# Performance work log

Hardware: AMD Instinct MI355X
Metric: run time of the kernel (lower is better)

## Reference

```python
import jax, jax.numpy as jnp
import numpy as np

B, DIM, N = 4, 256, 2048
DIM_CTX, M = 256, 2048
HEADS, DIM_HEAD = 8, 64
DIM_INNER = HEADS * DIM_HEAD  # 512
EPS = 1e-12  # matches F.normalize eps


def setup_inputs() -> dict:
    key = jax.random.key(0)
    ks = jax.random.split(key, 8)
    return {
        "fmap": jax.random.normal(ks[0], (B, DIM, N), dtype=jnp.float32),
        "context": jax.random.normal(ks[1], (B, DIM_CTX, M), dtype=jnp.float32),
        "mask": jax.random.randint(ks[2], (B, M), 0, 2) > 0,
        "gamma": jnp.ones((DIM, 1), dtype=jnp.float32),
        "gamma_ctx": jnp.ones((DIM_CTX, 1), dtype=jnp.float32),
        "Wq": jax.random.normal(ks[3], (DIM_INNER, DIM), dtype=jnp.float32) * (DIM ** -0.5),
        "Wkv": jax.random.normal(ks[4], (2 * DIM_INNER, DIM_CTX), dtype=jnp.float32) * (DIM_CTX ** -0.5),
        "Wout": jax.random.normal(ks[5], (DIM, DIM_INNER), dtype=jnp.float32) * (DIM_INNER ** -0.5),
    }


def channel_rmsnorm(x, gamma):
    # F.normalize(x, dim=1) * sqrt(dim) * gamma ; x: [b, c, n], gamma: [c, 1]
    scale = x.shape[1] ** 0.5
    norm = jnp.sqrt(jnp.sum(x * x, axis=1, keepdims=True))
    normed = x / jnp.maximum(norm, EPS)
    return normed * scale * gamma[None]


def reference(fmap, context, mask, gamma, gamma_ctx, Wq, Wkv, Wout):
    h, d = HEADS, DIM_HEAD
    attn_scale = d ** -0.5

    fmap_n = channel_rmsnorm(fmap, gamma)          # [b, dim, n]
    ctx_n = channel_rmsnorm(context, gamma_ctx)    # [b, dim_ctx, m]

    # 1x1 Conv1d == matmul over channels
    q = jnp.einsum('oc,bcn->bon', Wq, fmap_n)      # [b, h*d, n]
    kv = jnp.einsum('oc,bcm->bom', Wkv, ctx_n)     # [b, 2*h*d, m]
    k, v = jnp.split(kv, 2, axis=1)

    # [b, h*d, n] -> [b, h, n, d]
    def to_heads(t):
        b, _, nn = t.shape
        return t.reshape(b, h, d, nn).transpose(0, 1, 3, 2)

    q, k, v = to_heads(q), to_heads(k), to_heads(v)

    # L2-distance attention: sim = -||q_i - k_j||_2 * scale
    q2 = jnp.sum(q * q, axis=-1)                   # [b, h, n]
    k2 = jnp.sum(k * k, axis=-1)                   # [b, h, m]
    qk = jnp.einsum('bhid,bhjd->bhij', q, k)       # [b, h, n, m]
    d2 = jnp.maximum(q2[..., :, None] + k2[..., None, :] - 2.0 * qk, 0.0)
    dist = jnp.sqrt(jnp.maximum(d2, EPS))
    sim = -dist * attn_scale

    neg_max = -jnp.finfo(sim.dtype).max
    sim = jnp.where(mask[:, None, None, :], sim, neg_max)

    attn = jax.nn.softmax(sim, axis=-1)            # [b, h, n, m]
    out = jnp.einsum('bhij,bhjd->bhid', attn, v)   # [b, h, n, d]
    out = out.transpose(0, 1, 3, 2).reshape(out.shape[0], h * d, -1)  # [b, h*d, n]
    return jnp.einsum('oc,bcn->bon', Wout, out)    # [b, dim, n]
```

## Files before the change

### kernel.cpp

```cpp
#include <hip/hip_runtime.h>
#include <hip/hip_bf16.h>

#define B_ 4
#define DIM_ 256
#define N_ 2048
#define M_ 2048
#define HEADS_ 8
#define DHEAD_ 64
#define DINNER_ 512

typedef __attribute__((ext_vector_type(8))) short short8;
typedef __attribute__((ext_vector_type(4))) short short4v;
typedef __attribute__((ext_vector_type(4))) float floatx4;
typedef __attribute__((ext_vector_type(4))) _Float16 half4;
typedef __attribute__((ext_vector_type(8))) _Float16 half8;

#if defined(__has_builtin)
#if __has_builtin(__builtin_amdgcn_global_load_lds)
#define HAS_DMA 1
#endif
#endif

typedef __attribute__((address_space(1))) const void gvoid_t;
typedef __attribute__((address_space(3))) void lvoid_t;

#define CQ_ 0.18033688011112042f
#define NEG2CQ_ (-0.36067376022224084f)
#define EPS2_ 3.25213893e-14f

__device__ inline short bf16r(float x) {
  unsigned u = __float_as_uint(x);
  unsigned r = (u + 0x7fffu + ((u >> 16) & 1u)) >> 16;
  return (short)r;
}
__device__ inline float bf2f(short b) {
  return __uint_as_float(((unsigned)(unsigned short)b) << 16);
}

__global__ __launch_bounds__(256) void preproc_kernel(
    const float* __restrict__ Wq, const float* __restrict__ Wkv,
    const float* __restrict__ Wout, const float* __restrict__ gamma,
    const float* __restrict__ gctx, short* __restrict__ whi,
    short* __restrict__ wlo, const float* __restrict__ xf,
    const float* __restrict__ xc, short* __restrict__ xtf,
    short* __restrict__ xtc) {
  const int bid = blockIdx.x;
  const int tid = threadIdx.x;

  __shared__ float4 red4[16][16];
  __shared__ float scl[64];
  __shared__ float t[64][65];

  if (bid < 768) {
    const int y = bid >> 8;
    const int gsz[3] = {32768, 65536, 32768};
    const int goff[3] = {0, 131072, 393216};
    int gidx = (bid & 255) * 256 + tid;
    if (gidx >= gsz[y]) return;
    const float* W = (y == 0) ? Wq : (y == 1) ? Wkv : Wout;
    const int cmask = (y == 2) ? 511 : 255;
    int e0 = gidx * 4;
    int c = e0 & cmask;
    float4 wv = *(const float4*)&W[e0];
    if (y < 2) {
      const float* g = (y == 0) ? gamma : gctx;
      float4 g4 = *(const float4*)&g[c];
      wv.x *= g4.x; wv.y *= g4.y; wv.z *= g4.z; wv.w *= g4.w;
    }
    float vv[4] = {wv.x, wv.y, wv.z, wv.w};
    short4v hi, lo;
#pragma unroll
    for (int e = 0; e < 4; ++e) {
      short hb = bf16r(vv[e]);
      hi[e] = hb;
      lo[e] = bf16r(vv[e] - bf2f(hb));
    }
    *(short4v*)&whi[goff[y] + e0] = hi;
    *(short4v*)&wlo[goff[y] + e0] = lo;
    return;
  }

  const int cid = bid - 768;
  const int NN = 2048;
  const int z = cid >> 7;
  const int b = (cid >> 5) & 3;
  const int xblk = cid & 31;
  const float* x = (z == 0) ? xf : xc;
  short* xt = (z == 0) ? xtf : xtc;
  const int tx4 = tid & 15, tyc = tid >> 4;
  const int n0 = xblk * 64;
  const float* xb = x + (size_t)b * 256 * NN;

  float4 ssq4 = {0.f, 0.f, 0.f, 0.f};
  for (int c = tyc; c < 256; c += 16) {
    float4 v = *(const float4*)&xb[(size_t)c * NN + n0 + tx4 * 4];
    ssq4.x += v.x * v.x; ssq4.y += v.y * v.y;
    ssq4.z += v.z * v.z; ssq4.w += v.w * v.w;
  }
  red4[tyc][tx4] = ssq4;
  __syncthreads();
  if (tid < 16) {
    float4 s = red4[0][tid];
#pragma unroll
    for (int g = 1; g < 16; ++g) {
      float4 v = red4[g][tid];
      s.x += v.x; s.y += v.y; s.z += v.z; s.w += v.w;
    }
    scl[tid * 4 + 0] = 16.0f / fmaxf(sqrtf(s.x), 1e-12f);
    scl[tid * 4 + 1] = 16.0f / fmaxf(sqrtf(s.y), 1e-12f);
    scl[tid * 4 + 2] = 16.0f / fmaxf(sqrtf(s.z), 1e-12f);
    scl[tid * 4 + 3] = 16.0f / fmaxf(sqrtf(s.w), 1e-12f);
  }
  const int row = tid >> 2, cg = tid & 3;
  for (int c0 = 0; c0 < 256; c0 += 64) {
    __syncthreads();
    for (int cc = tyc; cc < 64; cc += 16) {
      float4 v = *(const float4*)&xb[(size_t)(c0 + cc) * NN + n0 + tx4 * 4];
      t[cc][tx4 * 4 + 0] = v.x;
      t[cc][tx4 * 4 + 1] = v.y;
      t[cc][tx4 * 4 + 2] = v.z;
      t[cc][tx4 * 4 + 3] = v.w;
    }
    __syncthreads();
    float sc = scl[row];
    short8 o0v, o1v;
#pragma unroll
    for (int e = 0; e < 8; ++e) {
      o0v[e] = bf16r(t[cg * 16 + e][row] * sc);
      o1v[e] = bf16r(t[cg * 16 + 8 + e][row] * sc);
    }
    size_t base = ((size_t)b * NN + n0 + row) * 256 + c0 + cg * 16;
    *(short8*)&xt[base] = o0v;
    *(short8*)&xt[base + 8] = o1v;
  }
}

__global__ __launch_bounds__(256) void qkv_gemm_kernel(
    const short* __restrict__ whi, const short* __restrict__ wlo,
    const short* __restrict__ fmap_t, const short* __restrict__ ctx_t,
    short* __restrict__ qb, short* __restrict__ kc, _Float16* __restrict__ vc,
    const int* __restrict__ maskp, float* __restrict__ k2m) {
  const int b = blockIdx.z;
  const int y = blockIdx.y;
  const bool isq = (y < 4);
  const int o0 = (isq ? y : y - 4) * 128;
  const int n0 = blockIdx.x * 128;
  const short* Wh = whi + (isq ? 0 : 131072);
  const short* Wl = wlo + (isq ? 0 : 131072);
  const short* Xt = isq ? fmap_t : ctx_t;

  const int tid = threadIdx.x;
  const int w = tid >> 6, l = tid & 63, quad = l >> 4, l15 = l & 15;
  const int wo = (w >> 1) * 64, wn = (w & 1) * 64;

  __shared__ __align__(16) char smem[36864];
  short* lWh = (short*)smem;
  short* lWl = (short*)(smem + 8192);
  short* lXb = (short*)(smem + 16384);

  floatx4 acc[4][4];
#pragma unroll
  for (int ot = 0; ot < 4; ++ot)
#pragma unroll
    for (int nt = 0; nt < 4; ++nt)
#pragma unroll
      for (int r = 0; r < 4; ++r) acc[ot][nt][r] = 0.f;

  const int drow = l >> 2;
  const int dslot = l & 3;

  for (int c0 = 0; c0 < 256; c0 += 32) {
    __syncthreads();
#pragma unroll
    for (int half = 0; half < 2; ++half) {
      int r0 = w * 32 + half * 16;
      int row = r0 + drow;
      int chunk = dslot ^ ((row >> 1) & 3);
      size_t wsrc = (size_t)(o0 + row) * 256 + c0 + chunk * 8;
      size_t xsrc = ((size_t)b * 2048 + n0 + row) * 256 + c0 + chunk * 8;
#ifdef HAS_DMA
      __builtin_amdgcn_global_load_lds((gvoid_t*)&Wh[wsrc],
                                       (lvoid_t*)&lWh[r0 * 32], 16, 0, 0);
      __builtin_amdgcn_global_load_lds((gvoid_t*)&Wl[wsrc],
                                       (lvoid_t*)&lWl[r0 * 32], 16, 0, 0);
      __builtin_amdgcn_global_load_lds((gvoid_t*)&Xt[xsrc],
                                       (lvoid_t*)&lXb[r0 * 32], 16, 0, 0);
#else
      *(short8*)&lWh[row * 32 + dslot * 8] = *(const short8*)&Wh[wsrc];
      *(short8*)&lWl[row * 32 + dslot * 8] = *(const short8*)&Wl[wsrc];
      *(short8*)&lXb[row * 32 + dslot * 8] = *(const short8*)&Xt[xsrc];
#endif
    }
    __syncthreads();

    short8 ah[4], al[4], bx[4];
#pragma unroll
    for (int ot = 0; ot < 4; ++ot) {
      int ar = wo + 16 * ot + l15;
      int sl = (quad ^ ((ar >> 1) & 3)) * 8;
      ah[ot] = *(const short8*)&lWh[ar * 32 + sl];
      al[ot] = *(const short8*)&lWl[ar * 32 + sl];
    }
#pragma unroll
    for (int nt = 0; nt < 4; ++nt) {
      int br = wn + 16 * nt + l15;
      int sl = (quad ^ ((br >> 1) & 3)) * 8;
      bx[nt] = *(const short8*)&lXb[br * 32 + sl];
    }
#pragma unroll
    for (int ot = 0; ot < 4; ++ot)
#pragma unroll
      for (int nt = 0; nt < 4; ++nt) {
        acc[ot][nt] =
            __builtin_amdgcn_mfma_f32_16x16x32_bf16(al[ot], bx[nt], acc[ot][nt], 0, 0, 0);
        acc[ot][nt] =
            __builtin_amdgcn_mfma_f32_16x16x32_bf16(ah[ot], bx[nt], acc[ot][nt], 0, 0, 0);
      }
  }

  if (isq) {
    __syncthreads();
    short (*qt)[72] = (short (*)[72])(smem + w * 9216);
#pragma unroll
    for (int nt = 0; nt < 4; ++nt)
#pragma unroll
      for (int ot = 0; ot < 4; ++ot) {
        short4v pk;
#pragma unroll
        for (int r = 0; r < 4; ++r) pk[r] = bf16r(CQ_ * acc[ot][nt][r]);
        *(short4v*)&qt[16 * nt + l15][16 * ot + 4 * quad] = pk;
      }
#pragma unroll
    for (int it = 0; it < 8; ++it) {
      int nr = 8 * it + (l >> 3);
      int c8 = (l & 7) * 8;
      *(short8*)&qb[((size_t)b * 2048 + n0 + wn + nr) * 512 + o0 + wo + c8] =
          *(const short8*)&qt[nr][c8];
    }
  } else if (o0 < 512) {
    const int head = (o0 + wo) >> 6;
    const int bh = b * 8 + head;
    const int chunk = (n0 + wn) >> 6;
    __syncthreads();
    short (*kt)[72] = (short (*)[72])(smem + w * 9216);
    float k2p[4] = {0.f, 0.f, 0.f, 0.f};
#pragma unroll
    for (int nt = 0; nt < 4; ++nt) {
      int mrow = 16 * nt + l15;
      int sw = mrow & 7;
#pragma unroll
      for (int ot = 0; ot < 4; ++ot) {
        int d0 = 16 * ot + 4 * quad;
        short4v pk;
#pragma unroll
        for (int r = 0; r < 4; ++r) {
          short pv = bf16r(NEG2CQ_ * acc[ot][nt][r]);
          pk[r] = pv;
          float kr = bf2f(pv);
          k2p[nt] += kr * kr;
        }
        *(short4v*)&kt[mrow][(((d0 >> 3) ^ sw) << 3) + (d0 & 7)] = pk;
      }
    }
    size_t tbase = ((size_t)bh * 32 + chunk) * 4096;
#pragma unroll
    for (int it = 0; it < 8; ++it) {
      int mr = 8 * it + (l >> 3);
      int c8 = (l & 7) * 8;
      *(short8*)&kc[tbase + mr * 64 + c8] = *(const short8*)&kt[mr][c8];
    }
#pragma unroll
    for (int nt = 0; nt < 4; ++nt) {
      float s = k2p[nt];
      s += __shfl_xor(s, 16);
      s += __shfl_xor(s, 32);
      if (quad == 0) {
        int m = n0 + wn + 16 * nt + l15;
        int mv = maskp[b * 2048 + m];
        k2m[(size_t)bh * 2048 + m] = mv ? 0.25f * s : __builtin_inff();
      }
    }
  } else {
    const int chv = o0 - 512 + wo;
    const int bh = b * 8 + (chv >> 6);
    const int chunk = (n0 + wn) >> 6;
    __syncthreads();
    _Float16 (*vt)[72] = (_Float16 (*)[72])(smem + w * 9216);
#pragma unroll
    for (int nt = 0; nt < 4; ++nt) {
      int jr = 16 * nt + l15;
      int jrem = jr & 31;
      int colp = 32 * (jr >> 5) + ((jrem >> 2) & 3) * 8 + (jrem >> 4) * 4 +
                 (jrem & 3);
#pragma unroll
      for (int ot = 0; ot < 4; ++ot)
#pragma unroll
        for (int r = 0; r < 4; ++r) {
          int drw = (16 * ot + 4 * quad + r) & 63;
          vt[drw][(((colp >> 3) ^ (drw & 7)) << 3) + (colp & 7)] =
              (_Float16)acc[ot][nt][r];
        }
    }
    size_t cbase = ((size_t)bh * 32 + chunk) * 4096;
#pragma unroll
    for (int it = 0; it < 8; ++it) {
      int dr = 8 * it + (l >> 3);
      int c8 = (l & 7) * 8;
      *(half8*)&vc[cbase + dr * 64 + c8] = *(const half8*)&vt[dr][c8];
    }
  }
}

__global__ __launch_bounds__(512, 8) void attn_kernel(
    const short* __restrict__ qb, const short* __restrict__ kc,
    const _Float16* __restrict__ vc, const float* __restrict__ k2m,
    short* __restrict__ attn_t) {
  const int bid = blockIdx.x;
  const int rr = bid & 7, qq = bid >> 3;
  const int bh = rr * 4 + (qq >> 5);
  const int iblk = qq & 31;
  const int h = bh & 7, b = bh >> 3;
  const int i0 = iblk * 64;

  const int tid = threadIdx.x;
  const int w = tid >> 6, l = tid & 63, quad = l >> 4, l15 = l & 15;
  const int wr = w >> 1, jh = w & 1;

  __shared__ __align__(16) short sbuf[2][2][4096];

  const short* qrow =
      qb + ((size_t)b * 2048 + i0 + 16 * wr + l15) * 512 + h * 64;
  const short* kcb = kc + (size_t)bh * 32 * 4096;
  const _Float16* vcb = vc + (size_t)bh * 32 * 4096;
  const float* k2b = k2m + (size_t)bh * 2048;

  short8 qa0 = *(const short8*)&qrow[8 * quad];
  short8 qa1 = *(const short8*)&qrow[32 + 8 * quad];
  float q2p = 0.f;
#pragma unroll
  for (int jj = 0; jj < 8; ++jj) {
    float f0 = bf2f(qa0[jj]), f1 = bf2f(qa1[jj]);
    q2p += f0 * f0 + f1 * f1;
  }
  q2p += __shfl_xor(q2p, 16);
  q2p += __shfl_xor(q2p, 32);
  const float q2c = q2p;

  floatx4 accO[4];
#pragma unroll
  for (int dt = 0; dt < 4; ++dt)
#pragma unroll
    for (int r = 0; r < 4; ++r) accO[dt][r] = 0.f;
  float lsum = 0.f;

  const int sx = l15 & 7;

  auto stage = [&](int c, int p) {
    const short* ks = kcb + (size_t)c * 4096 + w * 512 + l * 8;
    const _Float16* vs = vcb + (size_t)c * 4096 + w * 512 + l * 8;
#ifdef HAS_DMA
    __builtin_amdgcn_global_load_lds((gvoid_t*)ks,
                                     (lvoid_t*)&sbuf[0][p][w * 512], 16, 0, 0);
    __builtin_amdgcn_global_load_lds((gvoid_t*)vs,
                                     (lvoid_t*)&sbuf[1][p][w * 512], 16, 0, 0);
#else
    *(short8*)&sbuf[0][p][w * 512 + l * 8] = *(const short8*)ks;
    *(half8*)&((_Float16*)sbuf[1][p])[w * 512 + l * 8] = *(const half8*)vs;
#endif
  };

  stage(0, 0);
  for (int c = 0; c < 32; ++c) {
    __syncthreads();
    if (c < 31) stage(c + 1, (c + 1) & 1);
    const int p = c & 1;

    half8 pb;
#pragma unroll
    for (int jt = 0; jt < 2; ++jt) {
      float4 k2v = *(const float4*)&k2b[c * 64 + jh * 32 + 16 * jt + 4 * quad];
      const short* kr = &sbuf[0][p][(jh * 32 + 16 * jt + l15) * 64];
      short8 k0 = *(const short8*)&kr[(quad ^ sx) << 3];
      short8 k1 = *(const short8*)&kr[((quad + 4) ^ sx) << 3];
      floatx4 a;
      a[0] = q2c + k2v.x;
      a[1] = q2c + k2v.y;
      a[2] = q2c + k2v.z;
      a[3] = q2c + k2v.w;
      __builtin_amdgcn_s_setprio(1);
      a = __builtin_amdgcn_mfma_f32_16x16x32_bf16(k0, qa0, a, 0, 0, 0);
      a = __builtin_amdgcn_mfma_f32_16x16x32_bf16(k1, qa1, a, 0, 0, 0);
      __builtin_amdgcn_s_setprio(0);
#pragma unroll
      for (int r = 0; r < 4; ++r) {
        float s = __builtin_amdgcn_sqrtf(fmaxf(a[r], EPS2_));
        float pv = __builtin_amdgcn_exp2f(-s);
        lsum += pv;
        pb[4 * jt + r] = (_Float16)pv;
      }
    }

    __builtin_amdgcn_s_setprio(1);
#pragma unroll
    for (int dt = 0; dt < 4; ++dt) {
      const _Float16* vr = (const _Float16*)&sbuf[1][p][(16 * dt + l15) * 64];
      half8 hh = *(const half8*)&vr[((quad + 4 * jh) ^ sx) << 3];
      accO[dt] =
          __builtin_amdgcn_mfma_f32_16x16x32_f16(hh, pb, accO[dt], 0, 0, 0);
    }
    __builtin_amdgcn_s_setprio(0);
  }

  __syncthreads();
  float* scr = (float*)sbuf;
  const int sidx = (wr * 64 + l) * 17;
  if (jh) {
#pragma unroll
    for (int dt = 0; dt < 4; ++dt)
#pragma unroll
      for (int r = 0; r < 4; ++r) scr[sidx + dt * 4 + r] = accO[dt][r];
    scr[sidx + 16] = lsum;
  }
  __syncthreads();
  if (!jh) {
#pragma unroll
    for (int dt = 0; dt < 4; ++dt)
#pragma unroll
      for (int r = 0; r < 4; ++r) accO[dt][r] += scr[sidx + dt * 4 + r];
    lsum += scr[sidx + 16];
    lsum += __shfl_xor(lsum, 16);
    lsum += __shfl_xor(lsum, 32);
    float rl = 1.0f / lsum;
    size_t base = ((size_t)b * 2048 + i0 + 16 * wr + l15) * 512 + h * 64;
#pragma unroll
    for (int dt = 0; dt < 4; ++dt) {
      short4v pk;
#pragma unroll
      for (int r = 0; r < 4; ++r) pk[r] = bf16r(accO[dt][r] * rl);
      *(short4v*)&attn_t[base + 16 * dt + 4 * quad] = pk;
    }
  }
}

__global__ __launch_bounds__(256) void outproj_kernel(
    const short* __restrict__ whi, const short* __restrict__ wlo,
    const short* __restrict__ Xt, float* __restrict__ Yf) {
  const int b = blockIdx.z;
  const int n0 = blockIdx.x * 64;
  const int o0 = blockIdx.y * 64;
  const int tid = threadIdx.x;
  const int w = tid >> 6, l = tid & 63, quad = l >> 4, l15 = l & 15;
  const int wo = (w >> 1) * 32, wn = (w & 1) * 32;

  __shared__ __align__(16) short Wa[2][64][40];
  __shared__ __align__(16) short Xb[64][40];

  floatx4 acc[2][2];
#pragma unroll
  for (int ot = 0; ot < 2; ++ot)
#pragma unroll
    for (int nt = 0; nt < 2; ++nt)
#pragma unroll
      for (int r = 0; r < 4; ++r) acc[ot][nt][r] = 0.f;

  for (int c0 = 0; c0 < 512; c0 += 32) {
    __syncthreads();
    {
      int row = tid >> 2, sg = (tid & 3) * 8;
      size_t src = (size_t)(o0 + row) * 512 + c0 + sg;
      *(short8*)&Wa[0][row][sg] = *(const short8*)&whi[src];
      *(short8*)&Wa[1][row][sg] = *(const short8*)&wlo[src];
    }
    {
      int nn = tid >> 2, sg = (tid & 3) * 8;
      *(short8*)&Xb[nn][sg] =
          *(const short8*)&Xt[((size_t)b * 2048 + n0 + nn) * 512 + c0 + sg];
    }
    __syncthreads();

    short8 ah[2], al[2], bx[2];
#pragma unroll
    for (int ot = 0; ot < 2; ++ot) {
      ah[ot] = *(const short8*)&Wa[0][wo + 16 * ot + l15][8 * quad];
      al[ot] = *(const short8*)&Wa[1][wo + 16 * ot + l15][8 * quad];
    }
#pragma unroll
    for (int nt = 0; nt < 2; ++nt)
      bx[nt] = *(const short8*)&Xb[wn + 16 * nt + l15][8 * quad];
#pragma unroll
    for (int ot = 0; ot < 2; ++ot)
#pragma unroll
      for (int nt = 0; nt < 2; ++nt) {
        acc[ot][nt] =
            __builtin_amdgcn_mfma_f32_16x16x32_bf16(al[ot], bx[nt], acc[ot][nt], 0, 0, 0);
        acc[ot][nt] =
            __builtin_amdgcn_mfma_f32_16x16x32_bf16(ah[ot], bx[nt], acc[ot][nt], 0, 0, 0);
      }
  }

#pragma unroll
  for (int ot = 0; ot < 2; ++ot)
#pragma unroll
    for (int r = 0; r < 4; ++r) {
      int o = o0 + wo + 16 * ot + 4 * quad + r;
#pragma unroll
      for (int nt = 0; nt < 2; ++nt)
        Yf[((size_t)b * 256 + o) * 2048 + n0 + wn + 16 * nt + l15] =
            acc[ot][nt][r];
    }
}

extern "C" void kernel_launch(void* const* d_in, const int* in_sizes, int n_in,
                              void* d_out, int out_size, void* d_ws,
                              size_t ws_size, hipStream_t stream) {
  const float* fmap = (const float*)d_in[0];
  const float* context = (const float*)d_in[1];
  const int* mask = (const int*)d_in[2];
  const float* gamma = (const float*)d_in[3];
  const float* gamma_ctx = (const float*)d_in[4];
  const float* Wq = (const float*)d_in[5];
  const float* Wkv = (const float*)d_in[6];
  const float* Wout = (const float*)d_in[7];
  float* out = (float*)d_out;

  char* ws = (char*)d_ws;
  short* fmap_t = (short*)ws;
  short* ctx_t = fmap_t + 2097152;
  short* qb = ctx_t + 2097152;
  short* kc = qb + 4194304;
  _Float16* vc = (_Float16*)(kc + 4194304);
  short* attn_t = (short*)(vc + 4194304);
  float* k2m = (float*)(attn_t + 4194304);
  short* whi = (short*)(k2m + 65536);
  short* wlo = whi + 524288;

  preproc_kernel<<<dim3(1024), 256, 0, stream>>>(
      Wq, Wkv, Wout, gamma, gamma_ctx, whi, wlo, fmap, context, fmap_t, ctx_t);
  qkv_gemm_kernel<<<dim3(16, 12, B_), 256, 0, stream>>>(
      whi, wlo, fmap_t, ctx_t, qb, kc, vc, mask, k2m);
  attn_kernel<<<dim3(1024), 512, 0, stream>>>(qb, kc, vc, k2m, attn_t);
  outproj_kernel<<<dim3(32, 4, B_), 256, 0, stream>>>(whi + 393216,
                                                      wlo + 393216, attn_t,
                                                      out);
}
```

Baseline: 182.0 us.

## Double-buffer LDS staging in QKV and output projection GEMMs, vectorize output stores

Both projection GEMMs now use two LDS buffers, so the next K-slice is fetched while the current one feeds the MFMAs, and each iteration needs one barrier instead of two. The output projection switches to the async global-to-LDS DMA path with an XOR-swizzled layout in place of a padded array. Its epilogue goes through an LDS staging tile so results are written as float4 rows rather than scalar strided stores. The cost is more shared memory per block, which may lower occupancy, most for the QKV kernel at 48KB.

```diff
diff --git a/kernel.cpp b/kernel.cpp
--- a/kernel.cpp
+++ b/kernel.cpp
@@ -153,10 +153,7 @@
   const int w = tid >> 6, l = tid & 63, quad = l >> 4, l15 = l & 15;
   const int wo = (w >> 1) * 64, wn = (w & 1) * 64;
 
-  __shared__ __align__(16) char smem[36864];
-  short* lWh = (short*)smem;
-  short* lWl = (short*)(smem + 8192);
-  short* lXb = (short*)(smem + 16384);
+  __shared__ __align__(16) char smem[49152];
 
   floatx4 acc[4][4];
 #pragma unroll
@@ -166,32 +163,41 @@
 #pragma unroll
       for (int r = 0; r < 4; ++r) acc[ot][nt][r] = 0.f;
 
-  const int drow = l >> 2;
-  const int dslot = l & 3;
-
-  for (int c0 = 0; c0 < 256; c0 += 32) {
-    __syncthreads();
+  auto stageT = [&](int c0, int p) {
+    char* base = smem + p * 24576;
+    short* dWh = (short*)base;
+    short* dWl = (short*)(base + 8192);
+    short* dXb = (short*)(base + 16384);
 #pragma unroll
     for (int half = 0; half < 2; ++half) {
       int r0 = w * 32 + half * 16;
-      int row = r0 + drow;
-      int chunk = dslot ^ ((row >> 1) & 3);
+      int row = r0 + (l >> 2);
+      int chunk = (l & 3) ^ ((row >> 1) & 3);
       size_t wsrc = (size_t)(o0 + row) * 256 + c0 + chunk * 8;
       size_t xsrc = ((size_t)b * 2048 + n0 + row) * 256 + c0 + chunk * 8;
 #ifdef HAS_DMA
       __builtin_amdgcn_global_load_lds((gvoid_t*)&Wh[wsrc],
-                                       (lvoid_t*)&lWh[r0 * 32], 16, 0, 0);
+                                       (lvoid_t*)&dWh[r0 * 32], 16, 0, 0);
       __builtin_amdgcn_global_load_lds((gvoid_t*)&Wl[wsrc],
-                                       (lvoid_t*)&lWl[r0 * 32], 16, 0, 0);
+                                       (lvoid_t*)&dWl[r0 * 32], 16, 0, 0);
       __builtin_amdgcn_global_load_lds((gvoid_t*)&Xt[xsrc],
-                                       (lvoid_t*)&lXb[r0 * 32], 16, 0, 0);
+                                       (lvoid_t*)&dXb[r0 * 32], 16, 0, 0);
 #else
-      *(short8*)&lWh[row * 32 + dslot * 8] = *(const short8*)&Wh[wsrc];
-      *(short8*)&lWl[row * 32 + dslot * 8] = *(const short8*)&Wl[wsrc];
-      *(short8*)&lXb[row * 32 + dslot * 8] = *(const short8*)&Xt[xsrc];
+      *(short8*)&dWh[row * 32 + (l & 3) * 8] = *(const short8*)&Wh[wsrc];
+      *(short8*)&dWl[row * 32 + (l & 3) * 8] = *(const short8*)&Wl[wsrc];
+      *(short8*)&dXb[row * 32 + (l & 3) * 8] = *(const short8*)&Xt[xsrc];
 #endif
     }
-    __syncthreads();
+  };
+
+  stageT(0, 0);
+  for (int ci = 0; ci < 8; ++ci) {
+    __syncthreads();
+    if (ci < 7) stageT((ci + 1) * 32, (ci + 1) & 1);
+    const char* base = smem + (ci & 1) * 24576;
+    const short* lWh = (const short*)base;
+    const short* lWl = (const short*)(base + 8192);
+    const short* lXb = (const short*)(base + 16384);
 
     short8 ah[4], al[4], bx[4];
 #pragma unroll
@@ -452,8 +458,7 @@
   const int w = tid >> 6, l = tid & 63, quad = l >> 4, l15 = l & 15;
   const int wo = (w >> 1) * 32, wn = (w & 1) * 32;
 
-  __shared__ __align__(16) short Wa[2][64][40];
-  __shared__ __align__(16) short Xb[64][40];
+  __shared__ __align__(16) char smem[24576];
 
   floatx4 acc[2][2];
 #pragma unroll
@@ -463,30 +468,53 @@
 #pragma unroll
       for (int r = 0; r < 4; ++r) acc[ot][nt][r] = 0.f;
 
-  for (int c0 = 0; c0 < 512; c0 += 32) {
-    __syncthreads();
-    {
-      int row = tid >> 2, sg = (tid & 3) * 8;
-      size_t src = (size_t)(o0 + row) * 512 + c0 + sg;
-      *(short8*)&Wa[0][row][sg] = *(const short8*)&whi[src];
-      *(short8*)&Wa[1][row][sg] = *(const short8*)&wlo[src];
-    }
-    {
-      int nn = tid >> 2, sg = (tid & 3) * 8;
-      *(short8*)&Xb[nn][sg] =
-          *(const short8*)&Xt[((size_t)b * 2048 + n0 + nn) * 512 + c0 + sg];
-    }
-    __syncthreads();
+  auto stageT = [&](int c0, int p) {
+    char* base = smem + p * 12288;
+    short* dWh = (short*)base;
+    short* dWl = (short*)(base + 4096);
+    short* dXb = (short*)(base + 8192);
+    int r0 = w * 16;
+    int row = r0 + (l >> 2);
+    int chunk = (l & 3) ^ ((row >> 1) & 3);
+    size_t wsrc = (size_t)(o0 + row) * 512 + c0 + chunk * 8;
+    size_t xsrc = ((size_t)b * 2048 + n0 + row) * 512 + c0 + chunk * 8;
+#ifdef HAS_DMA
+    __builtin_amdgcn_global_load_lds((gvoid_t*)&whi[wsrc],
+                                     (lvoid_t*)&dWh[r0 * 32], 16, 0, 0);
+    __builtin_amdgcn_global_load_lds((gvoid_t*)&wlo[wsrc],
+                                     (lvoid_t*)&dWl[r0 * 32], 16, 0, 0);
+    __builtin_amdgcn_global_load_lds((gvoid_t*)&Xt[xsrc],
+                                     (lvoid_t*)&dXb[r0 * 32], 16, 0, 0);
+#else
+    *(short8*)&dWh[row * 32 + (l & 3) * 8] = *(const short8*)&whi[wsrc];
+    *(short8*)&dWl[row * 32 + (l & 3) * 8] = *(const short8*)&wlo[wsrc];
+    *(short8*)&dXb[row * 32 + (l & 3) * 8] = *(const short8*)&Xt[xsrc];
+#endif
+  };
+
+  stageT(0, 0);
+  for (int ci = 0; ci < 16; ++ci) {
+    __syncthreads();
+    if (ci < 15) stageT((ci + 1) * 32, (ci + 1) & 1);
+    const char* base = smem + (ci & 1) * 12288;
+    const short* lWh = (const short*)base;
+    const short* lWl = (const short*)(base + 4096);
+    const short* lXb = (const short*)(base + 8192);
 
     short8 ah[2], al[2], bx[2];
 #pragma unroll
     for (int ot = 0; ot < 2; ++ot) {
-      ah[ot] = *(const short8*)&Wa[0][wo + 16 * ot + l15][8 * quad];
-      al[ot] = *(const short8*)&Wa[1][wo + 16 * ot + l15][8 * quad];
-    }
-#pragma unroll
-    for (int nt = 0; nt < 2; ++nt)
-      bx[nt] = *(const short8*)&Xb[wn + 16 * nt + l15][8 * quad];
+      int ar = wo + 16 * ot + l15;
+      int sl = (quad ^ ((ar >> 1) & 3)) * 8;
+      ah[ot] = *(const short8*)&lWh[ar * 32 + sl];
+      al[ot] = *(const short8*)&lWl[ar * 32 + sl];
+    }
+#pragma unroll
+    for (int nt = 0; nt < 2; ++nt) {
+      int br = wn + 16 * nt + l15;
+      int sl = (quad ^ ((br >> 1) & 3)) * 8;
+      bx[nt] = *(const short8*)&lXb[br * 32 + sl];
+    }
 #pragma unroll
     for (int ot = 0; ot < 2; ++ot)
 #pragma unroll
@@ -498,16 +526,22 @@
       }
   }
 
+  __syncthreads();
+  float (*yt)[36] = (float (*)[36])(smem + w * 4608);
 #pragma unroll
   for (int ot = 0; ot < 2; ++ot)
 #pragma unroll
-    for (int r = 0; r < 4; ++r) {
-      int o = o0 + wo + 16 * ot + 4 * quad + r;
-#pragma unroll
-      for (int nt = 0; nt < 2; ++nt)
-        Yf[((size_t)b * 256 + o) * 2048 + n0 + wn + 16 * nt + l15] =
-            acc[ot][nt][r];
-    }
+    for (int nt = 0; nt < 2; ++nt)
+#pragma unroll
+      for (int r = 0; r < 4; ++r)
+        yt[16 * ot + 4 * quad + r][16 * nt + l15] = acc[ot][nt][r];
+#pragma unroll
+  for (int it = 0; it < 4; ++it) {
+    int orow = 8 * it + (l >> 3);
+    int c4 = (l & 7) * 4;
+    *(float4*)&Yf[((size_t)b * 256 + o0 + wo + orow) * 2048 + n0 + wn + c4] =
+        *(const float4*)&yt[orow][c4];
+  }
 }
 
 extern "C" void kernel_launch(void* const* d_in, const int* in_sizes, int n_in,
```

Measured after the change: 182.1 us. About the same (+0.1%).
